# Optimization experiments

Measured on AMD Instinct MI355X. Metric: run time of the kernel, lower is better.

The kernel has to match this reference:

```python
import jax, jax.numpy as jnp
import numpy as np

N_DROPOUT = 1      # init kwarg n_dropout
MIN_TOKENS = 10    # init kwarg min_tokens
# dynamic_dropout = False


def setup_inputs() -> dict:
    key = jax.random.key(0)
    k1, k2 = jax.random.split(key)
    B, S, V = 8192, 2048, 32000
    tokens = jax.random.randint(k1, (B, S), 1, V, dtype=jnp.int32)
    lengths = jax.random.randint(k2, (B,), 5, S + 1, dtype=jnp.int32)
    # contiguous prefix of positive token ids, 0-padded tail (as the module assumes)
    valid = jnp.arange(S, dtype=jnp.int32)[None, :] < lengths[:, None]
    input_ids = jnp.where(valid, tokens, 0)
    return {"input_ids": input_ids}


def reference(input_ids):
    # Vectorized equivalent of the per-row Python loop (training mode):
    # for every odd row with n_tokens >= MIN_TOKENS, zero N_DROPOUT random
    # token positions among the first n_tokens, then compact nonzeros left.
    B, S = input_ids.shape
    key = jax.random.key(42)

    n_tokens = jnp.sum(input_ids > 0, axis=1)  # [B]

    # random selection of N_DROPOUT distinct valid positions per row
    # (equivalent in distribution to randperm(n_tokens)[:N_DROPOUT])
    r = jax.random.uniform(key, (B, S))
    pos = jnp.arange(S)
    r = jnp.where(pos[None, :] < n_tokens[:, None], r, jnp.inf)
    _, drop_idx = jax.lax.top_k(-r, N_DROPOUT)  # [B, N_DROPOUT] smallest r
    drop_mask = jnp.zeros((B, S), dtype=bool).at[
        jnp.arange(B)[:, None], drop_idx
    ].set(True)

    apply_row = (jnp.arange(B) % 2 == 1) & (n_tokens >= MIN_TOKENS)  # [B]

    dropped = jnp.where(drop_mask & apply_row[:, None], 0, input_ids)

    # compaction: stable sort keys (zero-ness) -> nonzeros keep order, zeros go last
    order = jnp.argsort(dropped == 0, axis=1, stable=True)
    compacted = jnp.take_along_axis(dropped, order, axis=1)

    return jnp.where(apply_row[:, None], compacted, input_ids)
```

## Files before the change

### kernel.cpp

```cpp
#include <hip/hip_runtime.h>


constexpr int S = 2048;
constexpr int BLOCK = 256;
constexpr int ROWS_PER_BLOCK = 4;
constexpr int CHUNKS = S / 4 / 64;

__device__ __forceinline__ unsigned rotl32(unsigned x, int r) {
    return (x << r) | (x >> (32 - r));
}

__device__ __forceinline__ unsigned prng_bits(unsigned flat_idx) {
    const unsigned ks0 = 0u;
    const unsigned ks1 = 42u;
    const unsigned ks2 = 0x1BD11BDAu ^ ks0 ^ ks1;
    unsigned x0 = 0u + ks0;
    unsigned x1 = flat_idx + ks1;
#define TF_R4(a, b, c, d)                                   \
    x0 += x1; x1 = rotl32(x1, a); x1 ^= x0;                 \
    x0 += x1; x1 = rotl32(x1, b); x1 ^= x0;                 \
    x0 += x1; x1 = rotl32(x1, c); x1 ^= x0;                 \
    x0 += x1; x1 = rotl32(x1, d); x1 ^= x0;
    TF_R4(13, 15, 26, 6)   x0 += ks1; x1 += ks2 + 1u;
    TF_R4(17, 29, 16, 24)  x0 += ks2; x1 += ks0 + 2u;
    TF_R4(13, 15, 26, 6)   x0 += ks0; x1 += ks1 + 3u;
    TF_R4(17, 29, 16, 24)  x0 += ks1; x1 += ks2 + 4u;
    TF_R4(13, 15, 26, 6)   x0 += ks2; x1 += ks0 + 5u;
#undef TF_R4
    return x0 ^ x1;
}

__global__ __launch_bounds__(BLOCK) void random_dropout_kernel(
    const int* __restrict__ in, int* __restrict__ out) {
    const int wave = threadIdx.x >> 6;
    const int lane = threadIdx.x & 63;
    const int b = blockIdx.x * ROWS_PER_BLOCK + wave;
    const size_t base = (size_t)b * S;
    const int4* vin = (const int4*)(in + base);
    int4* vout = (int4*)(out + base);

    int4 v[CHUNKS];
    int cnt = 0;
#pragma unroll
    for (int k = 0; k < CHUNKS; k++) {
        v[k] = vin[lane + 64 * k];
        cnt += (v[k].x > 0) + (v[k].y > 0) + (v[k].z > 0) + (v[k].w > 0);
    }
#pragma unroll
    for (int off = 32; off; off >>= 1) cnt += __shfl_down(cnt, off, 64);
    const int ntok = __shfl(cnt, 0, 64);

    const bool apply = (b & 1) && (ntok >= 10);
    if (!apply) {
#pragma unroll
        for (int k = 0; k < CHUNKS; k++) vout[lane + 64 * k] = v[k];
        return;
    }

    unsigned long long best = ~0ull;
    const unsigned rowbase = (unsigned)b * (unsigned)S;
    for (int s = lane; s < ntok; s += 64) {
        const unsigned bits = prng_bits(rowbase + (unsigned)s);
        const unsigned long long comb =
            ((unsigned long long)(bits >> 9) << 11) | (unsigned)s;
        best = comb < best ? comb : best;
    }
#pragma unroll
    for (int off = 32; off; off >>= 1) {
        const unsigned long long o = __shfl_down(best, off, 64);
        best = o < best ? o : best;
    }
    const unsigned long long m = __shfl(best, 0, 64);
    const int drop = (int)(m & 0x7FFull);

    int nx[CHUNKS];
#pragma unroll
    for (int k = 0; k < CHUNKS; k++) {
        const int a = __shfl_down(v[k].x, 1, 64);
        const int bb = (k < CHUNKS - 1) ? __shfl(v[k + 1].x, 0, 64) : 0;
        nx[k] = (lane == 63) ? bb : a;
    }

#pragma unroll
    for (int k = 0; k < CHUNKS; k++) {
        const int j0 = 4 * (lane + 64 * k);
        int4 o;
        o.x = (j0 + 0 < drop) ? v[k].x : v[k].y;
        o.y = (j0 + 1 < drop) ? v[k].y : v[k].z;
        o.z = (j0 + 2 < drop) ? v[k].z : v[k].w;
        o.w = (j0 + 3 < drop) ? v[k].w : nx[k];
        vout[lane + 64 * k] = o;
    }
}

extern "C" void kernel_launch(void* const* d_in, const int* in_sizes, int n_in,
                              void* d_out, int out_size, void* d_ws, size_t ws_size,
                              hipStream_t stream) {
    const int* in = (const int*)d_in[0];
    int* out = (int*)d_out;
    const int total = in_sizes[0];
    const int B = total / S;
    random_dropout_kernel<<<B / ROWS_PER_BLOCK, BLOCK, 0, stream>>>(in, out);
}
```

Baseline: 118.0 us.

## Split even/odd rows across blocks and replace token count with position-9 check

```diff
diff --git a/kernel.cpp b/kernel.cpp
--- a/kernel.cpp
+++ b/kernel.cpp
@@ -3,7 +3,6 @@
 
 constexpr int S = 2048;
 constexpr int BLOCK = 256;
-constexpr int ROWS_PER_BLOCK = 4;
 constexpr int CHUNKS = S / 4 / 64;
 
 __device__ __forceinline__ unsigned rotl32(unsigned x, int r) {
@@ -30,27 +29,34 @@
     return x0 ^ x1;
 }
 
-__global__ __launch_bounds__(BLOCK) void random_dropout_kernel(
+__global__ __launch_bounds__(BLOCK, 8) void random_dropout_kernel(
     const int* __restrict__ in, int* __restrict__ out) {
     const int wave = threadIdx.x >> 6;
     const int lane = threadIdx.x & 63;
-    const int b = blockIdx.x * ROWS_PER_BLOCK + wave;
+    const int nb_even = (int)(gridDim.x >> 1);
+    const bool odd_block = (int)blockIdx.x >= nb_even;
+
+    const int slot = odd_block ? ((int)blockIdx.x - nb_even) : (int)blockIdx.x;
+    const int b = 2 * (4 * slot + wave) + (odd_block ? 1 : 0);
     const size_t base = (size_t)b * S;
     const int4* vin = (const int4*)(in + base);
     int4* vout = (int4*)(out + base);
 
+    if (!odd_block) {
+#pragma unroll
+        for (int k = 0; k < CHUNKS; k++) {
+            const int4 t = vin[lane + 64 * k];
+            vout[lane + 64 * k] = t;
+        }
+        return;
+    }
+
     int4 v[CHUNKS];
-    int cnt = 0;
 #pragma unroll
-    for (int k = 0; k < CHUNKS; k++) {
-        v[k] = vin[lane + 64 * k];
-        cnt += (v[k].x > 0) + (v[k].y > 0) + (v[k].z > 0) + (v[k].w > 0);
-    }
-#pragma unroll
-    for (int off = 32; off; off >>= 1) cnt += __shfl_down(cnt, off, 64);
-    const int ntok = __shfl(cnt, 0, 64);
+    for (int k = 0; k < CHUNKS; k++) v[k] = vin[lane + 64 * k];
 
-    const bool apply = (b & 1) && (ntok >= 10);
+    const bool apply = __shfl(v[0].y, 2, 64) > 0;
+
     if (!apply) {
 #pragma unroll
         for (int k = 0; k < CHUNKS; k++) vout[lane + 64 * k] = v[k];
@@ -59,19 +65,27 @@
 
     unsigned long long best = ~0ull;
     const unsigned rowbase = (unsigned)b * (unsigned)S;
-    for (int s = lane; s < ntok; s += 64) {
-        const unsigned bits = prng_bits(rowbase + (unsigned)s);
-        const unsigned long long comb =
-            ((unsigned long long)(bits >> 9) << 11) | (unsigned)s;
-        best = comb < best ? comb : best;
+#pragma unroll
+    for (int k = 0; k < CHUNKS; k++) {
+        const int s0 = 4 * (lane + 64 * k);
+        const int* e = (const int*)&v[k];
+#pragma unroll
+        for (int c = 0; c < 4; c++) {
+            if (e[c] > 0) {
+                const unsigned bits = prng_bits(rowbase + (unsigned)(s0 + c));
+                const unsigned long long comb =
+                    ((unsigned long long)(bits >> 9) << 11) |
+                    (unsigned)(s0 + c);
+                best = comb < best ? comb : best;
+            }
+        }
     }
 #pragma unroll
     for (int off = 32; off; off >>= 1) {
         const unsigned long long o = __shfl_down(best, off, 64);
         best = o < best ? o : best;
     }
-    const unsigned long long m = __shfl(best, 0, 64);
-    const int drop = (int)(m & 0x7FFull);
+    const int drop = (int)(__shfl(best, 0, 64) & 0x7FFull);
 
     int nx[CHUNKS];
 #pragma unroll
@@ -100,5 +114,5 @@
     int* out = (int*)d_out;
     const int total = in_sizes[0];
     const int B = total / S;
-    random_dropout_kernel<<<B / ROWS_PER_BLOCK, BLOCK, 0, stream>>>(in, out);
+    random_dropout_kernel<<<B / 4, BLOCK, 0, stream>>>(in, out);
 }
```

Result: no change. 116.8 us (-1.0%).
